# Kernel optimization log

Hardware: AMD Instinct MI355X
Metric: run time of the kernel (lower is better)

Reference implementation:

```python
import jax, jax.numpy as jnp
import numpy as np

N = 10000
E = 160000
D_IN, D_H = 512, 256


def _glorot(key, shape):
    fan_in, fan_out = shape[0], shape[1]
    lim = jnp.sqrt(6.0 / (fan_in + fan_out)).astype(jnp.float32)
    return jax.random.uniform(key, shape, jnp.float32, -lim, lim)


def setup_inputs() -> dict:
    key = jax.random.key(0)
    ks = jax.random.split(key, 12)
    x = jax.random.normal(ks[0], (N, D_IN), jnp.float32)
    edge_index = jax.random.randint(ks[1], (2, E), 0, N, jnp.int64)
    return {
        "x": x,
        "edge_index": edge_index,
        # SAGEConv: lin_l acts on aggregated neighbors (with bias), lin_r on root
        "W_l": _glorot(ks[2], (D_IN, D_H)),
        "b_l": jnp.zeros((D_H,), jnp.float32),
        "W_r": _glorot(ks[3], (D_IN, D_H)),
        "Wa": _glorot(ks[4], (256, 128)), "ba": jnp.zeros((128,), jnp.float32),
        "W1": _glorot(ks[5], (128, 64)),  "b1": jnp.zeros((64,), jnp.float32),
        "W2": _glorot(ks[6], (64, 32)),   "b2": jnp.zeros((32,), jnp.float32),
        "W3": _glorot(ks[7], (32, 3)),    "b3": jnp.zeros((3,), jnp.float32),
    }


def _sage_mean_aggr(x, edge_index):
    # PyG convention: message x_j = x[src], aggregated (mean) at dst
    src, dst = edge_index[0], edge_index[1]
    sums = jax.ops.segment_sum(x[src], dst, num_segments=N)          # [N, D_IN]
    cnt = jax.ops.segment_sum(jnp.ones((E,), x.dtype), dst, num_segments=N)
    return sums / jnp.maximum(cnt, 1.0)[:, None]


def _pairwise_l2(x):
    # cdist(x, x, p=2) via norm trick; zero-clamp for numerical safety
    sq = jnp.sum(x * x, axis=-1)                                      # [N]
    d2 = sq[:, None] + sq[None, :] - 2.0 * (x @ x.T)                  # [N, N]
    d2 = jnp.maximum(d2, 0.0)
    safe = jnp.where(d2 > 0, d2, 1.0)
    return jnp.where(d2 > 0, jnp.sqrt(safe), 0.0)


def reference(x, edge_index, W_l, b_l, W_r, Wa, ba, W1, b1, W2, b2, W3, b3):
    aggr = _sage_mean_aggr(x, edge_index)
    h = aggr @ W_l + b_l + x @ W_r                                    # SAGEConv out [N, 256]
    h = jax.nn.relu(h)
    h = jax.nn.relu(h @ Wa + ba)
    h = jax.nn.relu(h @ W1 + b1)
    h = jax.nn.relu(h @ W2 + b2)
    h = h @ W3 + b3                                                   # [N, 3]
    return _pairwise_l2(h)                                            # [N, N]
```

## Files before the change

### kernel.cpp

```cpp
#include <hip/hip_runtime.h>

#define N_NODES 10000
#define N_EDGES 160000

__global__ void count_kernel(const int* __restrict__ ei, int* __restrict__ deg) {
    int e = blockIdx.x * blockDim.x + threadIdx.x;
    if (e < N_EDGES) {
        int dst = ei[N_EDGES + e];
        atomicAdd(&deg[dst], 1);
    }
}

__global__ void scanA_kernel(const int* __restrict__ deg, int* __restrict__ row_start,
                             int* __restrict__ chunk_tot) {
    __shared__ int s[256];
    int c = blockIdx.x, tid = threadIdx.x;
    int i = c * 256 + tid;
    int v = (i < N_NODES) ? deg[i] : 0;
    s[tid] = v;
    __syncthreads();
    for (int off = 1; off < 256; off <<= 1) {
        int t = (tid >= off) ? s[tid - off] : 0;
        __syncthreads();
        s[tid] += t;
        __syncthreads();
    }
    if (i < N_NODES) row_start[i + 1] = s[tid];
    if (tid == 255) chunk_tot[c] = s[255];
}

__global__ void scanC_kernel(int* __restrict__ row_start, const int* __restrict__ chunk_tot) {
    int c = blockIdx.x, tid = threadIdx.x;
    int off = 0;
    for (int cc = 0; cc < c; ++cc) off += chunk_tot[cc];
    int i = c * 256 + tid;
    if (i < N_NODES) row_start[i + 1] += off;
    if (c == 0 && tid == 0) row_start[0] = 0;
}

__global__ void scatter_kernel(const int* __restrict__ ei, const int* __restrict__ row_start,
                               int* __restrict__ cursor, int* __restrict__ csr_src) {
    int e = blockIdx.x * blockDim.x + threadIdx.x;
    if (e < N_EDGES) {
        int src = ei[e];
        int dst = ei[N_EDGES + e];
        int p = atomicAdd(&cursor[dst], 1);
        csr_src[row_start[dst] + p] = src;
    }
}

__global__ __launch_bounds__(128) void aggr_kernel(const float* __restrict__ x,
                                                   const int* __restrict__ csr_src,
                                                   const int* __restrict__ row_start,
                                                   float* __restrict__ aggr) {
    int dst = blockIdx.x, tid = threadIdx.x;
    int beg = row_start[dst], end = row_start[dst + 1];
    float4 acc = make_float4(0.f, 0.f, 0.f, 0.f);
    for (int i = beg; i < end; ++i) {
        int src = csr_src[i];
        float4 v = *((const float4*)(x + (size_t)src * 512) + tid);
        acc.x += v.x; acc.y += v.y; acc.z += v.z; acc.w += v.w;
    }
    float inv = 1.0f / (float)max(end - beg, 1);
    float4 r = make_float4(acc.x * inv, acc.y * inv, acc.z * inv, acc.w * inv);
    *((float4*)(aggr + (size_t)dst * 512) + tid) = r;
}

template <bool RELU>
__global__ __launch_bounds__(256) void gemm_kernel(const float* __restrict__ A0,
                                                   const float* __restrict__ A1,
                                                   const float* __restrict__ B0,
                                                   const float* __restrict__ B1,
                                                   const float* __restrict__ bias,
                                                   float* __restrict__ C,
                                                   int M, int K, int N) {
    const int BK = 32;
    __shared__ float As[32][68];
    __shared__ float Bs[32][68];
    int tid = threadIdx.x;
    int rowbase = blockIdx.y * 64;
    int colbase = blockIdx.x * 64;
    float acc[4][4] = {};

    int nparts = (A1 != nullptr) ? 2 : 1;
    for (int part = 0; part < nparts; ++part) {
        const float* A = part ? A1 : A0;
        const float* B = part ? B1 : B0;
        for (int kt = 0; kt < K; kt += BK) {
            {
                int r = tid >> 3;
                int c4 = (tid & 7) * 4;
#pragma unroll
                for (int h = 0; h < 2; ++h) {
                    int row = rowbase + r + h * 32;
                    int arow = min(row, M - 1);
                    float4 v = *(const float4*)(A + (size_t)arow * K + kt + c4);
                    As[c4 + 0][r + h * 32] = v.x;
                    As[c4 + 1][r + h * 32] = v.y;
                    As[c4 + 2][r + h * 32] = v.z;
                    As[c4 + 3][r + h * 32] = v.w;
                }
            }
            {
                int kr = tid >> 4;
                int c4 = (tid & 15) * 4;
#pragma unroll
                for (int h = 0; h < 2; ++h) {
                    int k = kt + kr + h * 16;
                    int col = colbase + c4;
                    float4 v;
                    if (col + 4 <= N) {
                        v = *(const float4*)(B + (size_t)k * N + col);
                    } else {
                        v.x = (col + 0 < N) ? B[(size_t)k * N + col + 0] : 0.f;
                        v.y = (col + 1 < N) ? B[(size_t)k * N + col + 1] : 0.f;
                        v.z = (col + 2 < N) ? B[(size_t)k * N + col + 2] : 0.f;
                        v.w = (col + 3 < N) ? B[(size_t)k * N + col + 3] : 0.f;
                    }
                    *(float4*)&Bs[kr + h * 16][c4] = v;
                }
            }
            __syncthreads();
            int tm = (tid & 15) * 4;
            int tn = (tid >> 4) * 4;
#pragma unroll
            for (int kk = 0; kk < BK; ++kk) {
                float4 av = *(const float4*)&As[kk][tm];
                float4 bv = *(const float4*)&Bs[kk][tn];
                float a[4] = {av.x, av.y, av.z, av.w};
                float b[4] = {bv.x, bv.y, bv.z, bv.w};
#pragma unroll
                for (int i = 0; i < 4; ++i)
#pragma unroll
                    for (int j = 0; j < 4; ++j) acc[i][j] += a[i] * b[j];
            }
            __syncthreads();
        }
    }

    int tm = (tid & 15) * 4;
    int tn = (tid >> 4) * 4;
#pragma unroll
    for (int i = 0; i < 4; ++i) {
        int row = rowbase + tm + i;
        if (row >= M) continue;
#pragma unroll
        for (int j = 0; j < 4; ++j) {
            int col = colbase + tn + j;
            if (col >= N) continue;
            float v = acc[i][j] + bias[col];
            if (RELU) v = fmaxf(v, 0.f);
            C[(size_t)row * N + col] = v;
        }
    }
}

__global__ __launch_bounds__(256) void dist_kernel(const float* __restrict__ y,
                                                   float* __restrict__ out) {
    __shared__ float sa[192];
    __shared__ float sb[192];
    int rb = blockIdx.y * 64;
    int cb = blockIdx.x * 64;
    int tid = threadIdx.x;
    if (tid < 192) {
        int ga = rb * 3 + tid;
        sa[tid] = (ga < 3 * N_NODES) ? y[ga] : 0.f;
        int gb = cb * 3 + tid;
        sb[tid] = (gb < 3 * N_NODES) ? y[gb] : 0.f;
    }
    __syncthreads();
    int ty = tid >> 4;
    int tx = tid & 15;
    int c0 = tx * 4;
#pragma unroll
    for (int i = 0; i < 4; ++i) {
        int r = ty * 4 + i;
        int row = rb + r;
        if (row >= N_NODES) continue;
        float ax = sa[r * 3 + 0], ay = sa[r * 3 + 1], az = sa[r * 3 + 2];
        float res[4];
#pragma unroll
        for (int j = 0; j < 4; ++j) {
            int cc = c0 + j;
            float dx = ax - sb[cc * 3 + 0];
            float dy = ay - sb[cc * 3 + 1];
            float dz = az - sb[cc * 3 + 2];
            res[j] = sqrtf(dx * dx + dy * dy + dz * dz);
        }
        int col = cb + c0;
        size_t base = (size_t)row * N_NODES + col;
        if (col + 4 <= N_NODES) {
            *(float4*)(out + base) = make_float4(res[0], res[1], res[2], res[3]);
        } else {
#pragma unroll
            for (int j = 0; j < 4; ++j)
                if (col + j < N_NODES) out[base + j] = res[j];
        }
    }
}

extern "C" void kernel_launch(void* const* d_in, const int* in_sizes, int n_in,
                              void* d_out, int out_size, void* d_ws, size_t ws_size,
                              hipStream_t stream) {
    const float* x   = (const float*)d_in[0];
    const int*   ei  = (const int*)d_in[1];
    const float* W_l = (const float*)d_in[2];
    const float* b_l = (const float*)d_in[3];
    const float* W_r = (const float*)d_in[4];
    const float* Wa  = (const float*)d_in[5];
    const float* ba  = (const float*)d_in[6];
    const float* W1  = (const float*)d_in[7];
    const float* b1  = (const float*)d_in[8];
    const float* W2  = (const float*)d_in[9];
    const float* b2  = (const float*)d_in[10];
    const float* W3  = (const float*)d_in[11];
    const float* b3  = (const float*)d_in[12];

    float* out = (float*)d_out;
    float* aggr = out;
    float* h1   = out + 5120000;
    float* h2   = out + 7680000;
    float* h3   = out + 8960000;
    float* h4   = out + 9600000;

    float* y        = (float*)d_ws;
    int* deg        = (int*)d_ws + 30000;
    int* row_start  = (int*)d_ws + 40000;
    int* cursor     = (int*)d_ws + 50016;
    int* chunk_tot  = (int*)d_ws + 60016;
    int* csr_src    = (int*)d_ws + 60064;

    hipMemsetAsync(deg, 0, N_NODES * sizeof(int), stream);
    hipMemsetAsync(cursor, 0, N_NODES * sizeof(int), stream);

    count_kernel<<<(N_EDGES + 255) / 256, 256, 0, stream>>>(ei, deg);
    scanA_kernel<<<40, 256, 0, stream>>>(deg, row_start, chunk_tot);
    scanC_kernel<<<40, 256, 0, stream>>>(row_start, chunk_tot);
    scatter_kernel<<<(N_EDGES + 255) / 256, 256, 0, stream>>>(ei, row_start, cursor, csr_src);
    aggr_kernel<<<N_NODES, 128, 0, stream>>>(x, csr_src, row_start, aggr);

    dim3 b256(256);
    gemm_kernel<true><<<dim3(4, 157), b256, 0, stream>>>(aggr, x, W_l, W_r, b_l, h1, N_NODES, 512, 256);
    gemm_kernel<true><<<dim3(2, 157), b256, 0, stream>>>(h1, nullptr, Wa, nullptr, ba, h2, N_NODES, 256, 128);
    gemm_kernel<true><<<dim3(1, 157), b256, 0, stream>>>(h2, nullptr, W1, nullptr, b1, h3, N_NODES, 128, 64);
    gemm_kernel<true><<<dim3(1, 157), b256, 0, stream>>>(h3, nullptr, W2, nullptr, b2, h4, N_NODES, 64, 32);
    gemm_kernel<false><<<dim3(1, 157), b256, 0, stream>>>(h4, nullptr, W3, nullptr, b3, y, N_NODES, 32, 3);

    dist_kernel<<<dim3(157, 157), b256, 0, stream>>>(y, out);
}
```

Before: 698.4 us.

## Project features before aggregation and fuse mean-aggregation with bias and ReLU

Uses linearity of mean aggregation to compute x@W_l and x@W_r first with a new 128x128-tile register-prefetched GEMM. The neighbor gather then averages the projected features and is fused with the root term, bias and ReLU into a single kernel producing h1. This removes the separate 512-wide aggregation buffer and the two-part first GEMM. In exchange the gather reads 256-wide rows from a 512-stride intermediate, and the summation order changes slightly.

```diff
diff --git a/kernel.cpp b/kernel.cpp
--- a/kernel.cpp
+++ b/kernel.cpp
@@ -49,28 +49,123 @@
     }
 }
 
-__global__ __launch_bounds__(128) void aggr_kernel(const float* __restrict__ x,
-                                                   const int* __restrict__ csr_src,
-                                                   const int* __restrict__ row_start,
-                                                   float* __restrict__ aggr) {
-    int dst = blockIdx.x, tid = threadIdx.x;
+__global__ __launch_bounds__(256, 2) void zgemm_kernel(const float* __restrict__ x,
+                                                       const float* __restrict__ W_l,
+                                                       const float* __restrict__ W_r,
+                                                       float* __restrict__ Z) {
+    __shared__ float As[16][132];
+    __shared__ float Bs[16][132];
+    int tid = threadIdx.x;
+    int rowbase = blockIdx.y * 128;
+    int bx = blockIdx.x;
+    const float* B = (bx < 2) ? W_l : W_r;
+    int colb = (bx & 1) * 128;
+
+    int ar  = tid >> 2;
+    int ac4 = (tid & 3) << 2;
+    int bkr = tid >> 5;
+    int bc4 = (tid & 31) << 2;
+
+    int r0 = min(rowbase + ar, N_NODES - 1);
+    int r1 = min(rowbase + ar + 64, N_NODES - 1);
+    const float* a0p = x + (size_t)r0 * 512 + ac4;
+    const float* a1p = x + (size_t)r1 * 512 + ac4;
+    const float* b0p = B + (size_t)bkr * 256 + colb + bc4;
+    const float* b1p = B + (size_t)(bkr + 8) * 256 + colb + bc4;
+
+    float4 pa0 = *(const float4*)(a0p);
+    float4 pa1 = *(const float4*)(a1p);
+    float4 pb0 = *(const float4*)(b0p);
+    float4 pb1 = *(const float4*)(b1p);
+
+    As[ac4 + 0][ar] = pa0.x; As[ac4 + 1][ar] = pa0.y; As[ac4 + 2][ar] = pa0.z; As[ac4 + 3][ar] = pa0.w;
+    As[ac4 + 0][ar + 64] = pa1.x; As[ac4 + 1][ar + 64] = pa1.y; As[ac4 + 2][ar + 64] = pa1.z; As[ac4 + 3][ar + 64] = pa1.w;
+    *(float4*)&Bs[bkr][bc4] = pb0;
+    *(float4*)&Bs[bkr + 8][bc4] = pb1;
+    __syncthreads();
+
+    float acc[8][8] = {};
+    int tm = (tid & 15) << 3;
+    int tn = (tid >> 4) << 3;
+
+    for (int kt = 0; kt < 512; kt += 16) {
+        bool more = (kt + 16) < 512;
+        if (more) {
+            pa0 = *(const float4*)(a0p + kt + 16);
+            pa1 = *(const float4*)(a1p + kt + 16);
+            pb0 = *(const float4*)(b0p + (size_t)(kt + 16) * 256);
+            pb1 = *(const float4*)(b1p + (size_t)(kt + 16) * 256);
+        }
+#pragma unroll
+        for (int kk = 0; kk < 16; ++kk) {
+            float4 av0 = *(const float4*)&As[kk][tm];
+            float4 av1 = *(const float4*)&As[kk][tm + 4];
+            float4 bv0 = *(const float4*)&Bs[kk][tn];
+            float4 bv1 = *(const float4*)&Bs[kk][tn + 4];
+            float a[8] = {av0.x, av0.y, av0.z, av0.w, av1.x, av1.y, av1.z, av1.w};
+            float b[8] = {bv0.x, bv0.y, bv0.z, bv0.w, bv1.x, bv1.y, bv1.z, bv1.w};
+#pragma unroll
+            for (int i = 0; i < 8; ++i)
+#pragma unroll
+                for (int j = 0; j < 8; ++j) acc[i][j] += a[i] * b[j];
+        }
+        __syncthreads();
+        if (more) {
+            As[ac4 + 0][ar] = pa0.x; As[ac4 + 1][ar] = pa0.y; As[ac4 + 2][ar] = pa0.z; As[ac4 + 3][ar] = pa0.w;
+            As[ac4 + 0][ar + 64] = pa1.x; As[ac4 + 1][ar + 64] = pa1.y; As[ac4 + 2][ar + 64] = pa1.z; As[ac4 + 3][ar + 64] = pa1.w;
+            *(float4*)&Bs[bkr][bc4] = pb0;
+            *(float4*)&Bs[bkr + 8][bc4] = pb1;
+        }
+        __syncthreads();
+    }
+
+#pragma unroll
+    for (int i = 0; i < 8; ++i) {
+        int row = rowbase + tm + i;
+        if (row >= N_NODES) continue;
+        float* zr = Z + (size_t)row * 512 + bx * 128 + tn;
+        *(float4*)(zr)     = make_float4(acc[i][0], acc[i][1], acc[i][2], acc[i][3]);
+        *(float4*)(zr + 4) = make_float4(acc[i][4], acc[i][5], acc[i][6], acc[i][7]);
+    }
+}
+
+__global__ __launch_bounds__(256) void aggr_fused_kernel(const float* __restrict__ z,
+                                                         const int* __restrict__ csr_src,
+                                                         const int* __restrict__ row_start,
+                                                         const float* __restrict__ b_l,
+                                                         float* __restrict__ h1) {
+    int lane = threadIdx.x & 63;
+    int dst = blockIdx.x * 4 + (threadIdx.x >> 6);
     int beg = row_start[dst], end = row_start[dst + 1];
     float4 acc = make_float4(0.f, 0.f, 0.f, 0.f);
-    for (int i = beg; i < end; ++i) {
-        int src = csr_src[i];
-        float4 v = *((const float4*)(x + (size_t)src * 512) + tid);
-        acc.x += v.x; acc.y += v.y; acc.z += v.z; acc.w += v.w;
+    int i = beg;
+    for (; i + 1 < end; i += 2) {
+        int s0 = csr_src[i];
+        int s1 = csr_src[i + 1];
+        float4 v0 = *((const float4*)(z + (size_t)s0 * 512) + lane);
+        float4 v1 = *((const float4*)(z + (size_t)s1 * 512) + lane);
+        acc.x += v0.x + v1.x; acc.y += v0.y + v1.y;
+        acc.z += v0.z + v1.z; acc.w += v0.w + v1.w;
+    }
+    if (i < end) {
+        int s0 = csr_src[i];
+        float4 v0 = *((const float4*)(z + (size_t)s0 * 512) + lane);
+        acc.x += v0.x; acc.y += v0.y; acc.z += v0.z; acc.w += v0.w;
     }
     float inv = 1.0f / (float)max(end - beg, 1);
-    float4 r = make_float4(acc.x * inv, acc.y * inv, acc.z * inv, acc.w * inv);
-    *((float4*)(aggr + (size_t)dst * 512) + tid) = r;
+    float4 r = *((const float4*)(z + (size_t)dst * 512 + 256) + lane);
+    float4 bb = *((const float4*)b_l + lane);
+    float4 o;
+    o.x = fmaxf(fmaf(acc.x, inv, r.x + bb.x), 0.f);
+    o.y = fmaxf(fmaf(acc.y, inv, r.y + bb.y), 0.f);
+    o.z = fmaxf(fmaf(acc.z, inv, r.z + bb.z), 0.f);
+    o.w = fmaxf(fmaf(acc.w, inv, r.w + bb.w), 0.f);
+    *((float4*)(h1 + (size_t)dst * 256) + lane) = o;
 }
 
 template <bool RELU>
-__global__ __launch_bounds__(256) void gemm_kernel(const float* __restrict__ A0,
-                                                   const float* __restrict__ A1,
-                                                   const float* __restrict__ B0,
-                                                   const float* __restrict__ B1,
+__global__ __launch_bounds__(256) void gemm_kernel(const float* __restrict__ A,
+                                                   const float* __restrict__ B,
                                                    const float* __restrict__ bias,
                                                    float* __restrict__ C,
                                                    int M, int K, int N) {
@@ -82,60 +177,55 @@
     int colbase = blockIdx.x * 64;
     float acc[4][4] = {};
 
-    int nparts = (A1 != nullptr) ? 2 : 1;
-    for (int part = 0; part < nparts; ++part) {
-        const float* A = part ? A1 : A0;
-        const float* B = part ? B1 : B0;
-        for (int kt = 0; kt < K; kt += BK) {
-            {
-                int r = tid >> 3;
-                int c4 = (tid & 7) * 4;
-#pragma unroll
-                for (int h = 0; h < 2; ++h) {
-                    int row = rowbase + r + h * 32;
-                    int arow = min(row, M - 1);
-                    float4 v = *(const float4*)(A + (size_t)arow * K + kt + c4);
-                    As[c4 + 0][r + h * 32] = v.x;
-                    As[c4 + 1][r + h * 32] = v.y;
-                    As[c4 + 2][r + h * 32] = v.z;
-                    As[c4 + 3][r + h * 32] = v.w;
+    for (int kt = 0; kt < K; kt += BK) {
+        {
+            int r = tid >> 3;
+            int c4 = (tid & 7) * 4;
+#pragma unroll
+            for (int h = 0; h < 2; ++h) {
+                int row = rowbase + r + h * 32;
+                int arow = min(row, M - 1);
+                float4 v = *(const float4*)(A + (size_t)arow * K + kt + c4);
+                As[c4 + 0][r + h * 32] = v.x;
+                As[c4 + 1][r + h * 32] = v.y;
+                As[c4 + 2][r + h * 32] = v.z;
+                As[c4 + 3][r + h * 32] = v.w;
+            }
+        }
+        {
+            int kr = tid >> 4;
+            int c4 = (tid & 15) * 4;
+#pragma unroll
+            for (int h = 0; h < 2; ++h) {
+                int k = kt + kr + h * 16;
+                int col = colbase + c4;
+                float4 v;
+                if (col + 4 <= N) {
+                    v = *(const float4*)(B + (size_t)k * N + col);
+                } else {
+                    v.x = (col + 0 < N) ? B[(size_t)k * N + col + 0] : 0.f;
+                    v.y = (col + 1 < N) ? B[(size_t)k * N + col + 1] : 0.f;
+                    v.z = (col + 2 < N) ? B[(size_t)k * N + col + 2] : 0.f;
+                    v.w = (col + 3 < N) ? B[(size_t)k * N + col + 3] : 0.f;
                 }
+                *(float4*)&Bs[kr + h * 16][c4] = v;
             }
-            {
-                int kr = tid >> 4;
-                int c4 = (tid & 15) * 4;
-#pragma unroll
-                for (int h = 0; h < 2; ++h) {
-                    int k = kt + kr + h * 16;
-                    int col = colbase + c4;
-                    float4 v;
-                    if (col + 4 <= N) {
-                        v = *(const float4*)(B + (size_t)k * N + col);
-                    } else {
-                        v.x = (col + 0 < N) ? B[(size_t)k * N + col + 0] : 0.f;
-                        v.y = (col + 1 < N) ? B[(size_t)k * N + col + 1] : 0.f;
-                        v.z = (col + 2 < N) ? B[(size_t)k * N + col + 2] : 0.f;
-                        v.w = (col + 3 < N) ? B[(size_t)k * N + col + 3] : 0.f;
-                    }
-                    *(float4*)&Bs[kr + h * 16][c4] = v;
-                }
-            }
-            __syncthreads();
-            int tm = (tid & 15) * 4;
-            int tn = (tid >> 4) * 4;
-#pragma unroll
-            for (int kk = 0; kk < BK; ++kk) {
-                float4 av = *(const float4*)&As[kk][tm];
-                float4 bv = *(const float4*)&Bs[kk][tn];
-                float a[4] = {av.x, av.y, av.z, av.w};
-                float b[4] = {bv.x, bv.y, bv.z, bv.w};
-#pragma unroll
-                for (int i = 0; i < 4; ++i)
-#pragma unroll
-                    for (int j = 0; j < 4; ++j) acc[i][j] += a[i] * b[j];
-            }
-            __syncthreads();
-        }
+        }
+        __syncthreads();
+        int tm = (tid & 15) * 4;
+        int tn = (tid >> 4) * 4;
+#pragma unroll
+        for (int kk = 0; kk < BK; ++kk) {
+            float4 av = *(const float4*)&As[kk][tm];
+            float4 bv = *(const float4*)&Bs[kk][tn];
+            float a[4] = {av.x, av.y, av.z, av.w};
+            float b[4] = {bv.x, bv.y, bv.z, bv.w};
+#pragma unroll
+            for (int i = 0; i < 4; ++i)
+#pragma unroll
+                for (int j = 0; j < 4; ++j) acc[i][j] += a[i] * b[j];
+        }
+        __syncthreads();
     }
 
     int tm = (tid & 15) * 4;
@@ -217,7 +307,7 @@
     const float* b3  = (const float*)d_in[12];
 
     float* out = (float*)d_out;
-    float* aggr = out;
+    float* z    = out;
     float* h1   = out + 5120000;
     float* h2   = out + 7680000;
     float* h3   = out + 8960000;
@@ -233,18 +323,20 @@
     hipMemsetAsync(deg, 0, N_NODES * sizeof(int), stream);
     hipMemsetAsync(cursor, 0, N_NODES * sizeof(int), stream);
 
+    zgemm_kernel<<<dim3(4, 79), 256, 0, stream>>>(x, W_l, W_r, z);
+
     count_kernel<<<(N_EDGES + 255) / 256, 256, 0, stream>>>(ei, deg);
     scanA_kernel<<<40, 256, 0, stream>>>(deg, row_start, chunk_tot);
     scanC_kernel<<<40, 256, 0, stream>>>(row_start, chunk_tot);
     scatter_kernel<<<(N_EDGES + 255) / 256, 256, 0, stream>>>(ei, row_start, cursor, csr_src);
-    aggr_kernel<<<N_NODES, 128, 0, stream>>>(x, csr_src, row_start, aggr);
+
+    aggr_fused_kernel<<<2500, 256, 0, stream>>>(z, csr_src, row_start, b_l, h1);
 
     dim3 b256(256);
-    gemm_kernel<true><<<dim3(4, 157), b256, 0, stream>>>(aggr, x, W_l, W_r, b_l, h1, N_NODES, 512, 256);
-    gemm_kernel<true><<<dim3(2, 157), b256, 0, stream>>>(h1, nullptr, Wa, nullptr, ba, h2, N_NODES, 256, 128);
-    gemm_kernel<true><<<dim3(1, 157), b256, 0, stream>>>(h2, nullptr, W1, nullptr, b1, h3, N_NODES, 128, 64);
-    gemm_kernel<true><<<dim3(1, 157), b256, 0, stream>>>(h3, nullptr, W2, nullptr, b2, h4, N_NODES, 64, 32);
-    gemm_kernel<false><<<dim3(1, 157), b256, 0, stream>>>(h4, nullptr, W3, nullptr, b3, y, N_NODES, 32, 3);
+    gemm_kernel<true><<<dim3(2, 157), b256, 0, stream>>>(h1, Wa, ba, h2, N_NODES, 256, 128);
+    gemm_kernel<true><<<dim3(1, 157), b256, 0, stream>>>(h2, W1, b1, h3, N_NODES, 128, 64);
+    gemm_kernel<true><<<dim3(1, 157), b256, 0, stream>>>(h3, W2, b2, h4, N_NODES, 64, 32);
+    gemm_kernel<false><<<dim3(1, 157), b256, 0, stream>>>(h4, W3, b3, y, N_NODES, 32, 3);
 
     dist_kernel<<<dim3(157, 157), b256, 0, stream>>>(y, out);
 }
```

Result: slower. 1.049 ms (+50.2%).
